# Performance work log

Hardware: AMD Instinct MI355X
Metric: run time of the kernel (lower is better)

Reference implementation:

```python
import jax, jax.numpy as jnp
import numpy as np

N = 50000      # nodes
E = 400000     # edges
G = 128        # graphs in batch
D_NODE = 64
EDGE_DIM = 72
HEADS = 4
H0, H1, H2 = 128, 128, 64
NC = 2
NEG = 0.2      # GATConv leaky_relu negative_slope default
D1 = H2 + EDGE_DIM - 1  # ffn input dim = 135


def _p(k, shape, s=0.1):
    return jax.random.normal(k, shape, dtype=jnp.float32) * s


def setup_inputs() -> dict:
    key = jax.random.key(0)
    ks = jax.random.split(key, 24)
    x = jax.random.normal(ks[0], (N, D_NODE), dtype=jnp.float32)
    edge_index = jax.random.randint(ks[1], (2, E), 0, N)
    edge_attr = jax.random.uniform(ks[2], (E, EDGE_DIM), dtype=jnp.float32)
    batch = jnp.sort(jax.random.randint(ks[3], (N,), 0, G))
    return dict(
        x=x, edge_index=edge_index, edge_attr=edge_attr, batch=batch,
        # GATConv layer 1: in=D_NODE, out=H0, heads=HEADS, concat
        W1=_p(ks[4], (D_NODE, HEADS * H0)), We1=_p(ks[5], (EDGE_DIM, HEADS * H0)),
        as1=_p(ks[6], (HEADS, H0)), ad1=_p(ks[7], (HEADS, H0)), ae1=_p(ks[8], (HEADS, H0)),
        b1=jnp.zeros((HEADS * H0,), jnp.float32),
        # GATConv layer 2: in=HEADS*H0, out=H1, heads=HEADS, concat
        W2=_p(ks[9], (HEADS * H0, HEADS * H1)), We2=_p(ks[10], (EDGE_DIM, HEADS * H1)),
        as2=_p(ks[11], (HEADS, H1)), ad2=_p(ks[12], (HEADS, H1)), ae2=_p(ks[13], (HEADS, H1)),
        b2=jnp.zeros((HEADS * H1,), jnp.float32),
        # GATConv layer 3: in=HEADS*H1, out=H2, heads=1, concat=False
        W3=_p(ks[14], (HEADS * H1, H2)), We3=_p(ks[15], (EDGE_DIM, H2)),
        as3=_p(ks[16], (1, H2)), ad3=_p(ks[17], (1, H2)), ae3=_p(ks[18], (1, H2)),
        b3=jnp.zeros((H2,), jnp.float32),
        # ffn: Linear(135 -> 67), ReLU, Linear(67 -> 2), Softmax
        Wf1=_p(ks[19], (D1, D1 // 2)), bf1=jnp.zeros((D1 // 2,), jnp.float32),
        Wf2=_p(ks[20], (D1 // 2, NC)), bf2=jnp.zeros((NC,), jnp.float32),
    )


def _seg_softmax(s, seg, n):
    # numerically-stable softmax over segments (per-destination neighborhoods)
    m = jax.ops.segment_max(s, seg, num_segments=n)
    m = jnp.where(jnp.isfinite(m), m, 0.0)
    e = jnp.exp(s - m[seg])
    z = jax.ops.segment_sum(e, seg, num_segments=n)
    return e / (z[seg] + 1e-16)


def _gat(x, src, dst, eattr, W, We, a_s, a_d, a_e, b, heads, oc, concat):
    # PyG GATConv with edge_dim: shared src/dst projection, edge feats only in attention
    n = x.shape[0]
    xs = (x @ W).reshape(n, heads, oc)            # [N,H,C]
    ee = (eattr @ We).reshape(-1, heads, oc)      # [Ea,H,C]
    alpha = (xs * a_s).sum(-1)[src] + (xs * a_d).sum(-1)[dst] + (ee * a_e).sum(-1)
    alpha = jax.nn.leaky_relu(alpha, NEG)         # [Ea,H]
    alpha = _seg_softmax(alpha, dst, n)
    out = jax.ops.segment_sum(xs[src] * alpha[:, :, None], dst, num_segments=n)
    out = out.reshape(n, heads * oc) if concat else out.mean(axis=1)
    return out + b


def reference(x, edge_index, edge_attr, batch,
              W1, We1, as1, ad1, ae1, b1,
              W2, We2, as2, ad2, ae2, b2,
              W3, We3, as3, ad3, ae3, b3,
              Wf1, bf1, Wf2, bf2):
    src, dst = edge_index[0], edge_index[1]
    n = x.shape[0]
    # --- 1-gram feature vector: scatter-add edge_attr[:, :-1] by graph of src ---
    eb = batch[src]
    og = jax.ops.segment_sum(edge_attr[:, :-1], eb, num_segments=G)   # [G, EDGE_DIM-1]
    og = og / jnp.maximum(jnp.linalg.norm(og, axis=1, keepdims=True), 1e-12)
    # --- add self loops, edge_attr fill_value='mean' (mean over incoming edges) ---
    ones_e = jnp.ones((src.shape[0],), x.dtype)
    deg = jax.ops.segment_sum(ones_e, dst, num_segments=n)
    loop_attr = jax.ops.segment_sum(edge_attr, dst, num_segments=n) / jnp.maximum(deg, 1.0)[:, None]
    nodes = jnp.arange(n)
    src_a = jnp.concatenate([src, nodes])
    dst_a = jnp.concatenate([dst, nodes])
    ea = jnp.concatenate([edge_attr, loop_attr], axis=0)
    # --- GAT stack with ReLU activations ---
    h = jax.nn.relu(_gat(x, src_a, dst_a, ea, W1, We1, as1, ad1, ae1, b1, HEADS, H0, True))
    h = jax.nn.relu(_gat(h, src_a, dst_a, ea, W2, We2, as2, ad2, ae2, b2, HEADS, H1, True))
    h = jax.nn.relu(_gat(h, src_a, dst_a, ea, W3, We3, as3, ad3, ae3, b3, 1, H2, False))
    # --- global mean pool over graphs ---
    cnt = jax.ops.segment_sum(jnp.ones((n,), x.dtype), batch, num_segments=G)
    pooled = jax.ops.segment_sum(h, batch, num_segments=G) / jnp.maximum(cnt, 1.0)[:, None]
    # --- concat + ffn (dropout p=0 in eval) + softmax ---
    z = jnp.concatenate([pooled, og], axis=1)                         # [G, 135]
    z = jax.nn.relu(z @ Wf1 + bf1)
    return jax.nn.softmax(z @ Wf2 + bf2, axis=1)
```

## Files before the change

kernel.cpp:

```cpp
#include <hip/hip_runtime.h>

#define NNODES 50000
#define NEDGES 400000
#define NEA    450000
#define NG     128
#define DEGCAP 96
#define OGW    72

typedef unsigned short u16;
typedef unsigned int   u32;
typedef __attribute__((ext_vector_type(8))) short short8v;
typedef __attribute__((ext_vector_type(4))) float f32x4;

static inline int ceil_div(int a, int b){ return (a + b - 1)/b; }

__device__ __forceinline__ u16 f2bf(float f){
  u32 u = __builtin_bit_cast(u32, f);
  u = (u + 0x7fffu + ((u >> 16) & 1u)) >> 16;
  return (u16)u;
}
__device__ __forceinline__ float bf2f(u16 b){
  return __builtin_bit_cast(float, (u32)b << 16);
}
__device__ __forceinline__ void gload_lds16(const u16* g, u16* l){
  __builtin_amdgcn_global_load_lds((const __attribute__((address_space(1))) void*)g,
                                   (__attribute__((address_space(3))) void*)l, 16, 0, 0);
}

__global__ void k_prep(const float* __restrict__ x, u16* __restrict__ xb,
                       const float* __restrict__ W1, u16* __restrict__ Wt1,
                       const float* __restrict__ W2, u16* __restrict__ Wt2,
                       const float* __restrict__ W3, u16* __restrict__ Wt3,
                       const float* __restrict__ We1, const float* __restrict__ ae1,
                       const float* __restrict__ We2, const float* __restrict__ ae2,
                       const float* __restrict__ We3, const float* __restrict__ ae3,
                       float* __restrict__ veall){
  int i = blockIdx.x*blockDim.x + threadIdx.x;
  if (i < 800000){
    float4 v = ((const float4*)x)[i];
    ((ushort4*)xb)[i] = make_ushort4(f2bf(v.x), f2bf(v.y), f2bf(v.z), f2bf(v.w));
    return;
  }
  i -= 800000;
  if (i < 32768){
    int n = i >> 6, k = i & 63;
    Wt1[i] = f2bf(W1[(size_t)k*512 + n]);
    return;
  }
  i -= 32768;
  if (i < 262144){
    int n = i >> 9, k = i & 511;
    Wt2[i] = f2bf(W2[(size_t)k*512 + n]);
    return;
  }
  i -= 262144;
  if (i < 32768){
    int n = i >> 9, k = i & 511;
    Wt3[i] = f2bf(W3[(size_t)k*64 + n]);
    return;
  }
  i -= 32768;
  if (i < 648){
    const float* We; const float* ae; int H, C, basej, li;
    if (i < 288){ We = We1; ae = ae1; H = 4; C = 128; basej = 0; li = i; }
    else if (i < 576){ We = We2; ae = ae2; H = 4; C = 128; basej = 4; li = i - 288; }
    else { We = We3; ae = ae3; H = 1; C = 64; basej = 8; li = i - 576; }
    int k = li / H, h = li - k*H;
    const float* wrow = We + (size_t)k*H*C + (size_t)h*C;
    const float* arow = ae + (size_t)h*C;
    float s = 0.f;
    for (int c = 0; c < C; ++c) s += wrow[c]*arow[c];
    veall[k*9 + basej + h] = s;
  }
}

__global__ void k_deg_gb(const int* __restrict__ src, const int* __restrict__ dst,
                         const int* __restrict__ batch,
                         int* __restrict__ deg, int* __restrict__ gb, int* __restrict__ gcnt){
  __shared__ int h[NG];
  int t = threadIdx.x;
  if (t < NG) h[t] = 0;
  __syncthreads();
  int e = blockIdx.x*blockDim.x + t;
  if (e < NEDGES){
    atomicAdd(&deg[dst[e]], 1);
    int g = batch[src[e]];
    gb[e] = g;
    atomicAdd(&h[g], 1);
  }
  __syncthreads();
  if (t < NG && h[t]) atomicAdd(&gcnt[t], h[t]);
}

__global__ __launch_bounds__(1024) void k_scans(const int* __restrict__ deg, int* __restrict__ off,
                                                const int* __restrict__ gcnt, int* __restrict__ goff,
                                                int* __restrict__ gcur){
  __shared__ int s[1024];
  int t = threadIdx.x;
  if (blockIdx.x == 0){
    const int CH = (NNODES + 1023)/1024;
    int i0 = t*CH, i1 = min(i0 + CH, NNODES);
    int loc = 0;
    for (int i = i0; i < i1; ++i) loc += deg[i] + 1;
    s[t] = loc; __syncthreads();
    for (int o = 1; o < 1024; o <<= 1){
      int v = (t >= o) ? s[t-o] : 0;
      __syncthreads();
      s[t] += v;
      __syncthreads();
    }
    int excl = s[t] - loc;
    for (int i = i0; i < i1; ++i){ off[i] = excl; excl += deg[i] + 1; }
    if (t == 1023) off[NNODES] = s[1023];
  } else {
    int v = 0;
    if (t < NG){ v = gcnt[t]; s[t] = v; }
    __syncthreads();
    for (int o = 1; o < NG; o <<= 1){
      int x = 0;
      if (t < NG && t >= o) x = s[t-o];
      __syncthreads();
      if (t < NG) s[t] += x;
      __syncthreads();
    }
    if (t < NG){ goff[t] = s[t] - v; gcur[t] = s[t] - v; }
  }
}

__global__ void k_scatter(const int* __restrict__ src, const int* __restrict__ dst,
                          const int* __restrict__ gb, const int* __restrict__ off,
                          int* __restrict__ cnt, int* __restrict__ gcur,
                          int* __restrict__ csr_src, int* __restrict__ csr_eid,
                          int* __restrict__ sortedeid){
  __shared__ int lcnt[NG];
  __shared__ int lbase[NG];
  int t = threadIdx.x;
  int e = blockIdx.x*256 + t;
  if (t < NG) lcnt[t] = 0;
  __syncthreads();
  int g = -1, lr = 0;
  if (e < NEDGES){
    int d = dst[e];
    int p = off[d] + atomicAdd(&cnt[d], 1);
    csr_src[p] = src[e];
    csr_eid[p] = e;
    g = gb[e];
    lr = atomicAdd(&lcnt[g], 1);
  } else {
    int n2 = e - NEDGES;
    if (n2 < NNODES){
      int p = off[n2+1] - 1;
      csr_src[p] = n2;
      csr_eid[p] = -1;
    }
  }
  __syncthreads();
  if (t < NG && lcnt[t]) lbase[t] = atomicAdd(&gcur[t], lcnt[t]);
  __syncthreads();
  if (g >= 0) sortedeid[lbase[g] + lr] = e;
}

__global__ __launch_bounds__(256) void k_og2(const float* __restrict__ attr,
    const int* __restrict__ goff, const int* __restrict__ gcnt,
    const int* __restrict__ sortedeid, float* __restrict__ og){
  __shared__ float red[16][OGW];
  int g = blockIdx.x >> 4, chunk = blockIdx.x & 15;
  int lane = threadIdx.x & 63, w = threadIdx.x >> 6;
  int esub = lane >> 4, l16 = lane & 15;
  int slot = w*4 + esub;
  int beg = goff[g], cnt = gcnt[g];
  int cbeg = beg + ((cnt*chunk) >> 4);
  int cend = beg + ((cnt*(chunk+1)) >> 4);
  f32x4 acc  = {0.f,0.f,0.f,0.f};
  f32x4 acch = {0.f,0.f,0.f,0.f};
  for (int i0 = cbeg; i0 < cend; i0 += 32){
    int e1 = i0 + slot, e2 = i0 + 16 + slot;
    int id1 = (e1 < cend) ? sortedeid[e1] : -1;
    int id2 = (e2 < cend) ? sortedeid[e2] : -1;
    f32x4 v1 = {0.f,0.f,0.f,0.f}, v2 = {0.f,0.f,0.f,0.f};
    f32x4 h1 = {0.f,0.f,0.f,0.f}, h2 = {0.f,0.f,0.f,0.f};
    if (id1 >= 0){
      v1 = *(const f32x4*)(attr + (size_t)id1*72 + l16*4);
      if (l16 < 2) h1 = *(const f32x4*)(attr + (size_t)id1*72 + 64 + l16*4);
    }
    if (id2 >= 0){
      v2 = *(const f32x4*)(attr + (size_t)id2*72 + l16*4);
      if (l16 < 2) h2 = *(const f32x4*)(attr + (size_t)id2*72 + 64 + l16*4);
    }
    acc += v1; acc += v2;
    if (l16 < 2){ acch += h1; acch += h2; }
  }
  #pragma unroll
  for (int j = 0; j < 4; ++j) red[slot][l16*4 + j] = acc[j];
  if (l16 < 2){
    #pragma unroll
    for (int j = 0; j < 4; ++j) red[slot][64 + l16*4 + j] = acch[j];
  }
  __syncthreads();
  int t = threadIdx.x;
  if (t < 71){
    float s = 0.f;
    #pragma unroll
    for (int q = 0; q < 16; ++q) s += red[q][t];
    atomicAdd(&og[g*OGW + t], s);
  }
}

__global__ __launch_bounds__(256) void k_se_all(const float* __restrict__ attr,
    const float* __restrict__ veall, float* __restrict__ se){
  __shared__ float vel[72*9];
  for (int i = threadIdx.x; i < 72*9; i += blockDim.x) vel[i] = veall[i];
  __syncthreads();
  int e = blockIdx.x*blockDim.x + threadIdx.x;
  if (e >= NEDGES) return;
  const float4* row = (const float4*)(attr + (size_t)e*72);
  float s[9];
  #pragma unroll
  for (int j = 0; j < 9; ++j) s[j] = 0.f;
  #pragma unroll
  for (int kk = 0; kk < 18; ++kk){
    float4 a = row[kk];
    #pragma unroll
    for (int j = 0; j < 9; ++j)
      s[j] += a.x*vel[(kk*4+0)*9+j] + a.y*vel[(kk*4+1)*9+j]
            + a.z*vel[(kk*4+2)*9+j] + a.w*vel[(kk*4+3)*9+j];
  }
  #pragma unroll
  for (int j = 0; j < 9; ++j) se[(size_t)e*9+j] = s[j];
}

__global__ __launch_bounds__(256) void k_gemm128(const u16* __restrict__ A,
    const u16* __restrict__ Bt, u16* __restrict__ C, int M, int K,
    const float* __restrict__ a_s, const float* __restrict__ a_d,
    float* __restrict__ ssrc, float* __restrict__ sdst){
  __shared__ __align__(16) u16 smem[128*128];
  u16* As = smem;
  u16* Bs = smem + 128*64;
  __shared__ float s_ps[128][2];
  __shared__ float s_pd[128][2];
  const int tid = threadIdx.x;
  const int wid = tid >> 6, lane = tid & 63;
  const int l15 = lane & 15, kslot = lane >> 4;
  const int wr = wid >> 1, wc = wid & 1;
  const int h = blockIdx.x;
  const int m0 = blockIdx.y * 128, n0 = h * 128;
  const int Nn = 512;
  f32x4 acc[4][4];
  #pragma unroll
  for (int mi = 0; mi < 4; ++mi)
    #pragma unroll
    for (int ni = 0; ni < 4; ++ni)
      acc[mi][ni] = (f32x4){0.f,0.f,0.f,0.f};

  for (int kt = 0; kt < K; kt += 64){
    #pragma unroll
    for (int r = 0; r < 4; ++r){
      int chunk = (r*4 + wid)*64 + lane;
      int row = chunk >> 3, c8 = chunk & 7;
      int srcc = c8 ^ (row & 7);
      int grow = m0 + row; if (grow > M-1) grow = M-1;
      gload_lds16(A + (size_t)grow*K + kt + srcc*8, &As[chunk*8]);
    }
    #pragma unroll
    for (int r = 0; r < 4; ++r){
      int chunk = (r*4 + wid)*64 + lane;
      int row = chunk >> 3, c8 = chunk & 7;
      int srcc = c8 ^ (row & 7);
      gload_lds16(Bt + (size_t)(n0+row)*K + kt + srcc*8, &Bs[chunk*8]);
    }
    __syncthreads();
    #pragma unroll
    for (int s = 0; s < 2; ++s){
      short8v a[4], b[4];
      #pragma unroll
      for (int mi = 0; mi < 4; ++mi){
        int row = wr*64 + mi*16 + l15;
        a[mi] = *(const short8v*)(&As[row*64 + (((s*4 + kslot) ^ (row&7))*8)]);
      }
      #pragma unroll
      for (int ni = 0; ni < 4; ++ni){
        int col = wc*64 + ni*16 + l15;
        b[ni] = *(const short8v*)(&Bs[col*64 + (((s*4 + kslot) ^ (col&7))*8)]);
      }
      #pragma unroll
      for (int mi = 0; mi < 4; ++mi)
        #pragma unroll
        for (int ni = 0; ni < 4; ++ni)
          acc[mi][ni] = __builtin_amdgcn_mfma_f32_16x16x32_bf16(a[mi], b[ni], acc[mi][ni], 0, 0, 0);
    }
    __syncthreads();
  }
  float asv[4], adv[4];
  #pragma unroll
  for (int ni = 0; ni < 4; ++ni){
    int c = wc*64 + ni*16 + l15;
    asv[ni] = a_s[h*128 + c];
    adv[ni] = a_d[h*128 + c];
  }
  #pragma unroll
  for (int mi = 0; mi < 4; ++mi){
    #pragma unroll
    for (int r = 0; r < 4; ++r){
      int row_l = wr*64 + mi*16 + kslot*4 + r;
      float ps = 0.f, pd = 0.f;
      #pragma unroll
      for (int ni = 0; ni < 4; ++ni){
        float v = acc[mi][ni][r];
        smem[row_l*128 + wc*64 + ni*16 + l15] = f2bf(v);
        ps += v*asv[ni];
        pd += v*adv[ni];
      }
      #pragma unroll
      for (int m = 8; m >= 1; m >>= 1){ ps += __shfl_xor(ps,m); pd += __shfl_xor(pd,m); }
      if (l15 == 0){ s_ps[row_l][wc] = ps; s_pd[row_l][wc] = pd; }
    }
  }
  __syncthreads();
  #pragma unroll
  for (int i = 0; i < 8; ++i){
    int c = i*256 + tid;
    int row = c >> 4, c16 = c & 15;
    int grow = m0 + row;
    if (grow < M)
      *(uint4*)(C + (size_t)grow*Nn + n0 + c16*8) = *(const uint4*)(&smem[row*128 + c16*8]);
  }
  if (tid < 128){
    int grow = m0 + tid;
    if (grow < M){
      ssrc[grow*4 + h] = s_ps[tid][0] + s_ps[tid][1];
      sdst[grow*4 + h] = s_pd[tid][0] + s_pd[tid][1];
    }
  }
}

__global__ __launch_bounds__(256) void k_gemm64(const u16* __restrict__ A,
    const u16* __restrict__ Bt, float* __restrict__ C, int M,
    const float* __restrict__ a_s, const float* __restrict__ a_d,
    float* __restrict__ ssrc, float* __restrict__ sdst){
  __shared__ __align__(16) u16 As[64*64];
  __shared__ __align__(16) u16 Bs[64*64];
  const int tid = threadIdx.x;
  const int wid = tid >> 6, lane = tid & 63;
  const int l15 = lane & 15, kslot = lane >> 4;
  const int m0 = blockIdx.x * 64;
  f32x4 acc[4];
  #pragma unroll
  for (int ni = 0; ni < 4; ++ni) acc[ni] = (f32x4){0.f,0.f,0.f,0.f};
  for (int kt = 0; kt < 512; kt += 64){
    #pragma unroll
    for (int r = 0; r < 2; ++r){
      int chunk = r*256 + tid;
      int row = chunk >> 3, c8 = chunk & 7;
      int srcc = c8 ^ (row & 7);
      int grow = m0 + row; if (grow > M-1) grow = M-1;
      gload_lds16(A + (size_t)grow*512 + kt + srcc*8, &As[chunk*8]);
    }
    #pragma unroll
    for (int r = 0; r < 2; ++r){
      int chunk = r*256 + tid;
      int row = chunk >> 3, c8 = chunk & 7;
      int srcc = c8 ^ (row & 7);
      gload_lds16(Bt + (size_t)row*512 + kt + srcc*8, &Bs[chunk*8]);
    }
    __syncthreads();
    #pragma unroll
    for (int s = 0; s < 2; ++s){
      int row = wid*16 + l15;
      short8v a = *(const short8v*)(&As[row*64 + (((s*4 + kslot) ^ (row&7))*8)]);
      #pragma unroll
      for (int ni = 0; ni < 4; ++ni){
        int col = ni*16 + l15;
        short8v b = *(const short8v*)(&Bs[col*64 + (((s*4 + kslot) ^ (col&7))*8)]);
        acc[ni] = __builtin_amdgcn_mfma_f32_16x16x32_bf16(a, b, acc[ni], 0, 0, 0);
      }
    }
    __syncthreads();
  }
  #pragma unroll
  for (int r = 0; r < 4; ++r){
    int grow = m0 + wid*16 + kslot*4 + r;
    float ps = 0.f, pd = 0.f;
    #pragma unroll
    for (int ni = 0; ni < 4; ++ni){
      float v = acc[ni][r];
      if (grow < M) C[(size_t)grow*64 + ni*16 + l15] = v;
      int c = ni*16 + l15;
      ps += v*a_s[c];
      pd += v*a_d[c];
    }
    #pragma unroll
    for (int m = 8; m >= 1; m >>= 1){ ps += __shfl_xor(ps,m); pd += __shfl_xor(pd,m); }
    if (l15 == 0 && grow < M){ ssrc[grow] = ps; sdst[grow] = pd; }
  }
}

__global__ __launch_bounds__(256) void k_agg12(const u16* __restrict__ xs,
    const int* __restrict__ off, const int* __restrict__ csr_src, const int* __restrict__ csr_eid,
    const float* __restrict__ ssrc, const float* __restrict__ sdst,
    const float* __restrict__ se, int soff,
    const float* __restrict__ bias, u16* __restrict__ out){
  __shared__ float s_al[4][DEGCAP][4];
  __shared__ int   s_col[4][DEGCAP];
  int w = threadIdx.x >> 6, lane = threadIdx.x & 63;
  int n = blockIdx.x*4 + w;
  int beg = off[n];
  int deg = off[n+1] - beg;
  if (deg > DEGCAP) deg = DEGCAP;
  int es = lane >> 2, h = lane & 3;
  float sd = sdst[n*4+h];
  float sesum = 0.f;
  for (int e0 = 0; e0 < deg-1; e0 += 16){
    int e = e0 + es;
    if (e < deg-1){
      int col = csr_src[beg+e];
      int eid = csr_eid[beg+e];
      float sr = se[(size_t)eid*9+soff+h];
      sesum += sr;
      float s = ssrc[col*4+h] + sd + sr;
      s = (s > 0.f) ? s : 0.2f*s;
      s_al[w][e][h] = s;
      if (h == 0) s_col[w][e] = col;
    }
  }
  #pragma unroll
  for (int msk = 4; msk < 64; msk <<= 1) sesum += __shfl_xor(sesum, msk);
  if (es == 0){
    float slp = sesum / fmaxf((float)(deg-1), 1.0f);
    float s = ssrc[n*4+h] + sd + slp;
    s = (s > 0.f) ? s : 0.2f*s;
    s_al[w][deg-1][h] = s;
    if (h == 0) s_col[w][deg-1] = n;
  }
  float m = -1e30f;
  for (int e = es; e < deg; e += 16) m = fmaxf(m, s_al[w][e][h]);
  #pragma unroll
  for (int msk = 4; msk < 64; msk <<= 1) m = fmaxf(m, __shfl_xor(m, msk));
  float z = 0.f;
  for (int e = es; e < deg; e += 16){ float ex = expf(s_al[w][e][h]-m); s_al[w][e][h] = ex; z += ex; }
  #pragma unroll
  for (int msk = 4; msk < 64; msk <<= 1) z += __shfl_xor(z, msk);
  float inv = 1.0f/(z + 1e-16f);
  for (int e = es; e < deg; e += 16) s_al[w][e][h] *= inv;
  __syncthreads();
  int hh = lane >> 4;
  f32x4 accA = {0.f,0.f,0.f,0.f}, accB = {0.f,0.f,0.f,0.f};
  short8v v = *(const short8v*)(xs + (size_t)s_col[w][0]*512 + lane*8);
  for (int e = 0; e < deg; ++e){
    short8v vn = (short8v){0,0,0,0,0,0,0,0};
    if (e+1 < deg) vn = *(const short8v*)(xs + (size_t)s_col[w][e+1]*512 + lane*8);
    float a = s_al[w][e][hh];
    accA[0] += a*bf2f((u16)v[0]); accA[1] += a*bf2f((u16)v[1]);
    accA[2] += a*bf2f((u16)v[2]); accA[3] += a*bf2f((u16)v[3]);
    accB[0] += a*bf2f((u16)v[4]); accB[1] += a*bf2f((u16)v[5]);
    accB[2] += a*bf2f((u16)v[6]); accB[3] += a*bf2f((u16)v[7]);
    v = vn;
  }
  f32x4 b0 = *(const f32x4*)(bias + lane*8);
  f32x4 b1 = *(const f32x4*)(bias + lane*8 + 4);
  short8v res;
  res[0] = (short)f2bf(fmaxf(accA[0]+b0[0], 0.f));
  res[1] = (short)f2bf(fmaxf(accA[1]+b0[1], 0.f));
  res[2] = (short)f2bf(fmaxf(accA[2]+b0[2], 0.f));
  res[3] = (short)f2bf(fmaxf(accA[3]+b0[3], 0.f));
  res[4] = (short)f2bf(fmaxf(accB[0]+b1[0], 0.f));
  res[5] = (short)f2bf(fmaxf(accB[1]+b1[1], 0.f));
  res[6] = (short)f2bf(fmaxf(accB[2]+b1[2], 0.f));
  res[7] = (short)f2bf(fmaxf(accB[3]+b1[3], 0.f));
  *(short8v*)(out + (size_t)n*512 + lane*8) = res;
}

__global__ __launch_bounds__(256) void k_agg3(const float* __restrict__ xs,
    const int* __restrict__ off, const int* __restrict__ csr_src, const int* __restrict__ csr_eid,
    const float* __restrict__ ssrc, const float* __restrict__ sdst,
    const float* __restrict__ se,
    const float* __restrict__ bias, float* __restrict__ out){
  __shared__ float s_al[4][DEGCAP];
  __shared__ int   s_col[4][DEGCAP];
  int w = threadIdx.x >> 6, lane = threadIdx.x & 63;
  int n = blockIdx.x*4 + w;
  int beg = off[n];
  int deg = off[n+1] - beg;
  if (deg > DEGCAP) deg = DEGCAP;
  float sd = sdst[n];
  float sesum = 0.f;
  for (int e0 = 0; e0 < deg-1; e0 += 64){
    int e = e0 + lane;
    if (e < deg-1){
      int col = csr_src[beg+e];
      int eid = csr_eid[beg+e];
      float sr = se[(size_t)eid*9+8];
      sesum += sr;
      float s = ssrc[col] + sd + sr;
      s = (s > 0.f) ? s : 0.2f*s;
      s_al[w][e] = s;
      s_col[w][e] = col;
    }
  }
  #pragma unroll
  for (int msk = 1; msk < 64; msk <<= 1) sesum += __shfl_xor(sesum, msk);
  if (lane == 0){
    float slp = sesum / fmaxf((float)(deg-1), 1.0f);
    float s = ssrc[n] + sd + slp;
    s = (s > 0.f) ? s : 0.2f*s;
    s_al[w][deg-1] = s;
    s_col[w][deg-1] = n;
  }
  float m = -1e30f;
  for (int e = lane; e < deg; e += 64) m = fmaxf(m, s_al[w][e]);
  #pragma unroll
  for (int msk = 1; msk < 64; msk <<= 1) m = fmaxf(m, __shfl_xor(m, msk));
  float z = 0.f;
  for (int e = lane; e < deg; e += 64){ float ex = expf(s_al[w][e]-m); s_al[w][e] = ex; z += ex; }
  #pragma unroll
  for (int msk = 1; msk < 64; msk <<= 1) z += __shfl_xor(z, msk);
  float inv = 1.0f/(z + 1e-16f);
  for (int e = lane; e < deg; e += 64) s_al[w][e] *= inv;
  __syncthreads();
  float acc = 0.f;
  float v = xs[(size_t)s_col[w][0]*64 + lane];
  for (int e = 0; e < deg; ++e){
    float vn = 0.f;
    if (e+1 < deg) vn = xs[(size_t)s_col[w][e+1]*64 + lane];
    acc += s_al[w][e] * v;
    v = vn;
  }
  out[(size_t)n*64 + lane] = fmaxf(acc + bias[lane], 0.f);
}

__global__ __launch_bounds__(64) void k_pool(const float* __restrict__ h, const int* __restrict__ batch,
                                             float* __restrict__ pooled, int* __restrict__ cntg){
  int l = threadIdx.x;
  int start = blockIdx.x * 128;
  if (start >= NNODES) return;
  int endn = min(start + 128, NNODES);
  float acc = 0.f;
  int curg = batch[start];
  int run = 0;
  for (int n = start; n < endn; ++n){
    int g = batch[n];
    if (g != curg){
      atomicAdd(&pooled[curg*64+l], acc);
      if (l == 0) atomicAdd(&cntg[curg], run);
      acc = 0.f; run = 0; curg = g;
    }
    acc += h[(size_t)n*64 + l];
    ++run;
  }
  atomicAdd(&pooled[curg*64+l], acc);
  if (l == 0) atomicAdd(&cntg[curg], run);
}

__global__ void k_ffn(const float* __restrict__ pooled, const int* __restrict__ cntg,
                      const float* __restrict__ og,
                      const float* __restrict__ Wf1, const float* __restrict__ bf1,
                      const float* __restrict__ Wf2, const float* __restrict__ bf2,
                      float* __restrict__ out){
  __shared__ float z[135];
  __shared__ float z1[67];
  __shared__ float o2[2];
  int g = blockIdx.x, t = threadIdx.x;
  if (t < 64) z[t] = pooled[g*64+t] * (1.0f/fmaxf((float)cntg[g], 1.0f));
  else if (t < 135) z[t] = og[g*OGW + (t-64)];
  __syncthreads();
  if (t == 0){
    float s = 0.f;
    for (int k = 0; k < 71; ++k) s += z[64+k]*z[64+k];
    float scale = 1.0f / fmaxf(sqrtf(s), 1e-12f);
    for (int k = 0; k < 71; ++k) z[64+k] *= scale;
  }
  __syncthreads();
  if (t < 67){
    float s = bf1[t];
    for (int d = 0; d < 135; ++d) s += z[d]*Wf1[d*67+t];
    z1[t] = fmaxf(s, 0.f);
  }
  __syncthreads();
  if (t < 2){
    float s = bf2[t];
    for (int j = 0; j < 67; ++j) s += z1[j]*Wf2[j*2+t];
    o2[t] = s;
  }
  __syncthreads();
  if (t == 0){
    float m = fmaxf(o2[0], o2[1]);
    float e0 = expf(o2[0]-m), e1 = expf(o2[1]-m);
    float inv = 1.0f/(e0+e1);
    out[g*2+0] = e0*inv;
    out[g*2+1] = e1*inv;
  }
}

extern "C" void kernel_launch(void* const* d_in, const int* in_sizes, int n_in,
                              void* d_out, int out_size, void* d_ws, size_t ws_size,
                              hipStream_t stream){
  const float* x     = (const float*)d_in[0];
  const int*   ei    = (const int*)d_in[1];
  const float* eattr = (const float*)d_in[2];
  const int*   batch = (const int*)d_in[3];
  const float* W1  = (const float*)d_in[4];
  const float* We1 = (const float*)d_in[5];
  const float* as1 = (const float*)d_in[6];
  const float* ad1 = (const float*)d_in[7];
  const float* ae1 = (const float*)d_in[8];
  const float* b1  = (const float*)d_in[9];
  const float* W2  = (const float*)d_in[10];
  const float* We2 = (const float*)d_in[11];
  const float* as2 = (const float*)d_in[12];
  const float* ad2 = (const float*)d_in[13];
  const float* ae2 = (const float*)d_in[14];
  const float* b2  = (const float*)d_in[15];
  const float* W3  = (const float*)d_in[16];
  const float* We3 = (const float*)d_in[17];
  const float* as3 = (const float*)d_in[18];
  const float* ad3 = (const float*)d_in[19];
  const float* ae3 = (const float*)d_in[20];
  const float* b3  = (const float*)d_in[21];
  const float* Wf1 = (const float*)d_in[22];
  const float* bf1 = (const float*)d_in[23];
  const float* Wf2 = (const float*)d_in[24];
  const float* bf2 = (const float*)d_in[25];
  (void)in_sizes; (void)n_in; (void)out_size; (void)ws_size;
  const int* src = ei;
  const int* dst = ei + NEDGES;
  float* out = (float*)d_out;

  char* base = (char*)d_ws;
  size_t woff = 0;
  auto alloc = [&](size_t bytes)->char*{
    char* p = base + woff;
    woff += (bytes + 255) & ~(size_t)255;
    return p;
  };
  u16*   xsb    = (u16*)  alloc((size_t)NNODES*512*2);
  u16*   hb     = (u16*)  alloc((size_t)NNODES*512*2);
  float* xs3    = (float*)alloc((size_t)NNODES*64*4);
  float* h3     = (float*)alloc((size_t)NNODES*64*4);
  u16*   xb     = (u16*)  alloc((size_t)NNODES*64*2);
  u16*   Wt1    = (u16*)  alloc((size_t)512*64*2);
  u16*   Wt2    = (u16*)  alloc((size_t)512*512*2);
  u16*   Wt3    = (u16*)  alloc((size_t)64*512*2);
  float* se     = (float*)alloc((size_t)NEDGES*9*4);
  float* ssrc   = (float*)alloc((size_t)NNODES*4*4);
  float* sdst   = (float*)alloc((size_t)NNODES*4*4);
  float* veall  = (float*)alloc(72*9*4);
  int*   gb     = (int*)alloc((size_t)NEDGES*4);
  int*   csroff = (int*)alloc((size_t)(NNODES+1)*4);
  int*   csrsrc = (int*)alloc((size_t)NEA*4);
  int*   csreid = (int*)alloc((size_t)NEA*4);
  int*   goff   = (int*)alloc(NG*4);
  int*   gcur   = (int*)alloc(NG*4);
  int*   sortedeid = (int*)alloc((size_t)NEDGES*4);
  size_t z0 = woff;
  int*   deg    = (int*)alloc((size_t)NNODES*4);
  int*   cnt    = (int*)alloc((size_t)NNODES*4);
  int*   gcnt   = (int*)alloc(NG*4);
  float* og     = (float*)alloc((size_t)NG*OGW*4);
  float* pooled = (float*)alloc((size_t)NG*64*4);
  int*   cntg   = (int*)alloc((size_t)NG*4);
  size_t zlen = woff - z0;

  hipMemsetAsync(base + z0, 0, zlen, stream);

  k_prep<<<ceil_div(800000+32768+262144+32768+648,256),256,0,stream>>>(
      x, xb, W1, Wt1, W2, Wt2, W3, Wt3, We1, ae1, We2, ae2, We3, ae3, veall);

  k_deg_gb <<<ceil_div(NEDGES,256),256,0,stream>>>(src, dst, batch, deg, gb, gcnt);
  k_scans  <<<2,1024,0,stream>>>(deg, csroff, gcnt, goff, gcur);
  k_scatter<<<ceil_div(NEDGES+NNODES,256),256,0,stream>>>(src, dst, gb, csroff, cnt, gcur,
                                                          csrsrc, csreid, sortedeid);

  k_og2   <<<NG*16,256,0,stream>>>(eattr, goff, gcnt, sortedeid, og);
  k_se_all<<<ceil_div(NEDGES,256),256,0,stream>>>(eattr, veall, se);

  dim3 g128(4, ceil_div(NNODES,128));

  k_gemm128<<<g128,256,0,stream>>>(xb, Wt1, xsb, NNODES, 64, as1, ad1, ssrc, sdst);
  k_agg12<<<NNODES/4,256,0,stream>>>(xsb, csroff, csrsrc, csreid, ssrc, sdst, se, 0, b1, hb);

  k_gemm128<<<g128,256,0,stream>>>(hb, Wt2, xsb, NNODES, 512, as2, ad2, ssrc, sdst);
  k_agg12<<<NNODES/4,256,0,stream>>>(xsb, csroff, csrsrc, csreid, ssrc, sdst, se, 4, b2, hb);

  k_gemm64<<<ceil_div(NNODES,64),256,0,stream>>>(hb, Wt3, xs3, NNODES, as3, ad3, ssrc, sdst);
  k_agg3<<<NNODES/4,256,0,stream>>>(xs3, csroff, csrsrc, csreid, ssrc, sdst, se, b3, h3);

  k_pool<<<ceil_div(NNODES,128),64,0,stream>>>(h3, batch, pooled, cntg);
  k_ffn <<<NG,192,0,stream>>>(pooled, cntg, og, Wf1, bf1, Wf2, bf2, out);
}
```

Measured before the change: 609.1 us.

## Store edge scores in CSR order, bf16 layer-3 features, batched gathers in aggregation

The per-edge attention score projections are now written directly in CSR order, split into per-layer arrays. This removes the csr_eid indirection and the scattered 9-wide reads in each aggregation kernel. The layer-3 GEMM now emits bf16 features via an LDS staging pass, halving the bytes gathered in k_agg3. The aggregation loops are unrolled by 4 edges with padded neighbour lists and use __expf, exposing more independent gathers in flight. In exchange, the padding costs extra loads of the node's own row, and layer 3 loses some precision.

```diff
diff --git a/kernel.cpp b/kernel.cpp
--- a/kernel.cpp
+++ b/kernel.cpp
@@ -19,9 +19,8 @@
   u = (u + 0x7fffu + ((u >> 16) & 1u)) >> 16;
   return (u16)u;
 }
-__device__ __forceinline__ float bf2f(u16 b){
-  return __builtin_bit_cast(float, (u32)b << 16);
-}
+__device__ __forceinline__ float bfLO(u32 q){ return __builtin_bit_cast(float, q << 16); }
+__device__ __forceinline__ float bfHI(u32 q){ return __builtin_bit_cast(float, q & 0xffff0000u); }
 __device__ __forceinline__ void gload_lds16(const u16* g, u16* l){
   __builtin_amdgcn_global_load_lds((const __attribute__((address_space(1))) void*)g,
                                    (__attribute__((address_space(3))) void*)l, 16, 0, 0);
@@ -130,7 +129,7 @@
 __global__ void k_scatter(const int* __restrict__ src, const int* __restrict__ dst,
                           const int* __restrict__ gb, const int* __restrict__ off,
                           int* __restrict__ cnt, int* __restrict__ gcur,
-                          int* __restrict__ csr_src, int* __restrict__ csr_eid,
+                          int* __restrict__ csr_src, int* __restrict__ edgepos,
                           int* __restrict__ sortedeid){
   __shared__ int lcnt[NG];
   __shared__ int lbase[NG];
@@ -143,7 +142,7 @@
     int d = dst[e];
     int p = off[d] + atomicAdd(&cnt[d], 1);
     csr_src[p] = src[e];
-    csr_eid[p] = e;
+    edgepos[e] = p;
     g = gb[e];
     lr = atomicAdd(&lcnt[g], 1);
   } else {
@@ -151,7 +150,6 @@
     if (n2 < NNODES){
       int p = off[n2+1] - 1;
       csr_src[p] = n2;
-      csr_eid[p] = -1;
     }
   }
   __syncthreads();
@@ -207,7 +205,8 @@
 }
 
 __global__ __launch_bounds__(256) void k_se_all(const float* __restrict__ attr,
-    const float* __restrict__ veall, float* __restrict__ se){
+    const int* __restrict__ edgepos, const float* __restrict__ veall,
+    float* __restrict__ se1, float* __restrict__ se2, float* __restrict__ se3){
   __shared__ float vel[72*9];
   for (int i = threadIdx.x; i < 72*9; i += blockDim.x) vel[i] = veall[i];
   __syncthreads();
@@ -225,8 +224,10 @@
       s[j] += a.x*vel[(kk*4+0)*9+j] + a.y*vel[(kk*4+1)*9+j]
             + a.z*vel[(kk*4+2)*9+j] + a.w*vel[(kk*4+3)*9+j];
   }
-  #pragma unroll
-  for (int j = 0; j < 9; ++j) se[(size_t)e*9+j] = s[j];
+  int p = edgepos[e];
+  *(float4*)(se1 + (size_t)p*4) = make_float4(s[0], s[1], s[2], s[3]);
+  *(float4*)(se2 + (size_t)p*4) = make_float4(s[4], s[5], s[6], s[7]);
+  se3[p] = s[8];
 }
 
 __global__ __launch_bounds__(256) void k_gemm128(const u16* __restrict__ A,
@@ -334,7 +335,7 @@
 }
 
 __global__ __launch_bounds__(256) void k_gemm64(const u16* __restrict__ A,
-    const u16* __restrict__ Bt, float* __restrict__ C, int M,
+    const u16* __restrict__ Bt, u16* __restrict__ C, int M,
     const float* __restrict__ a_s, const float* __restrict__ a_d,
     float* __restrict__ ssrc, float* __restrict__ sdst){
   __shared__ __align__(16) u16 As[64*64];
@@ -378,13 +379,14 @@
   }
   #pragma unroll
   for (int r = 0; r < 4; ++r){
-    int grow = m0 + wid*16 + kslot*4 + r;
+    int row_l = wid*16 + kslot*4 + r;
+    int grow = m0 + row_l;
     float ps = 0.f, pd = 0.f;
     #pragma unroll
     for (int ni = 0; ni < 4; ++ni){
       float v = acc[ni][r];
-      if (grow < M) C[(size_t)grow*64 + ni*16 + l15] = v;
       int c = ni*16 + l15;
+      As[row_l*64 + c] = f2bf(v);
       ps += v*a_s[c];
       pd += v*a_d[c];
     }
@@ -392,12 +394,21 @@
     for (int m = 8; m >= 1; m >>= 1){ ps += __shfl_xor(ps,m); pd += __shfl_xor(pd,m); }
     if (l15 == 0 && grow < M){ ssrc[grow] = ps; sdst[grow] = pd; }
   }
+  __syncthreads();
+  #pragma unroll
+  for (int i = 0; i < 2; ++i){
+    int c = i*256 + tid;
+    int row = c >> 3, c8 = c & 7;
+    int grow = m0 + row;
+    if (grow < M)
+      *(uint4*)(C + (size_t)grow*64 + c8*8) = *(const uint4*)(&As[row*64 + c8*8]);
+  }
 }
 
 __global__ __launch_bounds__(256) void k_agg12(const u16* __restrict__ xs,
-    const int* __restrict__ off, const int* __restrict__ csr_src, const int* __restrict__ csr_eid,
+    const int* __restrict__ off, const int* __restrict__ csr_src,
     const float* __restrict__ ssrc, const float* __restrict__ sdst,
-    const float* __restrict__ se, int soff,
+    const float* __restrict__ sep,
     const float* __restrict__ bias, u16* __restrict__ out){
   __shared__ float s_al[4][DEGCAP][4];
   __shared__ int   s_col[4][DEGCAP];
@@ -413,8 +424,7 @@
     int e = e0 + es;
     if (e < deg-1){
       int col = csr_src[beg+e];
-      int eid = csr_eid[beg+e];
-      float sr = se[(size_t)eid*9+soff+h];
+      float sr = sep[(size_t)(beg+e)*4 + h];
       sesum += sr;
       float s = ssrc[col*4+h] + sd + sr;
       s = (s > 0.f) ? s : 0.2f*s;
@@ -436,24 +446,32 @@
   #pragma unroll
   for (int msk = 4; msk < 64; msk <<= 1) m = fmaxf(m, __shfl_xor(m, msk));
   float z = 0.f;
-  for (int e = es; e < deg; e += 16){ float ex = expf(s_al[w][e][h]-m); s_al[w][e][h] = ex; z += ex; }
+  for (int e = es; e < deg; e += 16){ float ex = __expf(s_al[w][e][h]-m); s_al[w][e][h] = ex; z += ex; }
   #pragma unroll
   for (int msk = 4; msk < 64; msk <<= 1) z += __shfl_xor(z, msk);
   float inv = 1.0f/(z + 1e-16f);
   for (int e = es; e < deg; e += 16) s_al[w][e][h] *= inv;
+  int degR = (deg + 3) & ~3;
+  for (int e = deg + es; e < degR; e += 16){ s_al[w][e][h] = 0.f; if (h == 0) s_col[w][e] = n; }
   __syncthreads();
   int hh = lane >> 4;
   f32x4 accA = {0.f,0.f,0.f,0.f}, accB = {0.f,0.f,0.f,0.f};
-  short8v v = *(const short8v*)(xs + (size_t)s_col[w][0]*512 + lane*8);
-  for (int e = 0; e < deg; ++e){
-    short8v vn = (short8v){0,0,0,0,0,0,0,0};
-    if (e+1 < deg) vn = *(const short8v*)(xs + (size_t)s_col[w][e+1]*512 + lane*8);
-    float a = s_al[w][e][hh];
-    accA[0] += a*bf2f((u16)v[0]); accA[1] += a*bf2f((u16)v[1]);
-    accA[2] += a*bf2f((u16)v[2]); accA[3] += a*bf2f((u16)v[3]);
-    accB[0] += a*bf2f((u16)v[4]); accB[1] += a*bf2f((u16)v[5]);
-    accB[2] += a*bf2f((u16)v[6]); accB[3] += a*bf2f((u16)v[7]);
-    v = vn;
+  for (int e = 0; e < degR; e += 4){
+    int c0 = s_col[w][e+0], c1 = s_col[w][e+1], c2 = s_col[w][e+2], c3 = s_col[w][e+3];
+    uint4 q0 = *(const uint4*)(xs + (size_t)c0*512 + lane*8);
+    uint4 q1 = *(const uint4*)(xs + (size_t)c1*512 + lane*8);
+    uint4 q2 = *(const uint4*)(xs + (size_t)c2*512 + lane*8);
+    uint4 q3 = *(const uint4*)(xs + (size_t)c3*512 + lane*8);
+    float a0 = s_al[w][e+0][hh], a1 = s_al[w][e+1][hh];
+    float a2 = s_al[w][e+2][hh], a3 = s_al[w][e+3][hh];
+    accA[0] += a0*bfLO(q0.x) + a1*bfLO(q1.x) + a2*bfLO(q2.x) + a3*bfLO(q3.x);
+    accA[1] += a0*bfHI(q0.x) + a1*bfHI(q1.x) + a2*bfHI(q2.x) + a3*bfHI(q3.x);
+    accA[2] += a0*bfLO(q0.y) + a1*bfLO(q1.y) + a2*bfLO(q2.y) + a3*bfLO(q3.y);
+    accA[3] += a0*bfHI(q0.y) + a1*bfHI(q1.y) + a2*bfHI(q2.y) + a3*bfHI(q3.y);
+    accB[0] += a0*bfLO(q0.z) + a1*bfLO(q1.z) + a2*bfLO(q2.z) + a3*bfLO(q3.z);
+    accB[1] += a0*bfHI(q0.z) + a1*bfHI(q1.z) + a2*bfHI(q2.z) + a3*bfHI(q3.z);
+    accB[2] += a0*bfLO(q0.w) + a1*bfLO(q1.w) + a2*bfLO(q2.w) + a3*bfLO(q3.w);
+    accB[3] += a0*bfHI(q0.w) + a1*bfHI(q1.w) + a2*bfHI(q2.w) + a3*bfHI(q3.w);
   }
   f32x4 b0 = *(const f32x4*)(bias + lane*8);
   f32x4 b1 = *(const f32x4*)(bias + lane*8 + 4);
@@ -469,10 +487,10 @@
   *(short8v*)(out + (size_t)n*512 + lane*8) = res;
 }
 
-__global__ __launch_bounds__(256) void k_agg3(const float* __restrict__ xs,
-    const int* __restrict__ off, const int* __restrict__ csr_src, const int* __restrict__ csr_eid,
+__global__ __launch_bounds__(256) void k_agg3(const u16* __restrict__ xs,
+    const int* __restrict__ off, const int* __restrict__ csr_src,
     const float* __restrict__ ssrc, const float* __restrict__ sdst,
-    const float* __restrict__ se,
+    const float* __restrict__ se3,
     const float* __restrict__ bias, float* __restrict__ out){
   __shared__ float s_al[4][DEGCAP];
   __shared__ int   s_col[4][DEGCAP];
@@ -487,8 +505,7 @@
     int e = e0 + lane;
     if (e < deg-1){
       int col = csr_src[beg+e];
-      int eid = csr_eid[beg+e];
-      float sr = se[(size_t)eid*9+8];
+      float sr = se3[beg+e];
       sesum += sr;
       float s = ssrc[col] + sd + sr;
       s = (s > 0.f) ? s : 0.2f*s;
@@ -510,21 +527,32 @@
   #pragma unroll
   for (int msk = 1; msk < 64; msk <<= 1) m = fmaxf(m, __shfl_xor(m, msk));
   float z = 0.f;
-  for (int e = lane; e < deg; e += 64){ float ex = expf(s_al[w][e]-m); s_al[w][e] = ex; z += ex; }
+  for (int e = lane; e < deg; e += 64){ float ex = __expf(s_al[w][e]-m); s_al[w][e] = ex; z += ex; }
   #pragma unroll
   for (int msk = 1; msk < 64; msk <<= 1) z += __shfl_xor(z, msk);
   float inv = 1.0f/(z + 1e-16f);
   for (int e = lane; e < deg; e += 64) s_al[w][e] *= inv;
-  __syncthreads();
-  float acc = 0.f;
-  float v = xs[(size_t)s_col[w][0]*64 + lane];
-  for (int e = 0; e < deg; ++e){
-    float vn = 0.f;
-    if (e+1 < deg) vn = xs[(size_t)s_col[w][e+1]*64 + lane];
-    acc += s_al[w][e] * v;
-    v = vn;
-  }
-  out[(size_t)n*64 + lane] = fmaxf(acc + bias[lane], 0.f);
+  int degR = (deg + 3) & ~3;
+  for (int e = deg + lane; e < degR; e += 64){ s_al[w][e] = 0.f; s_col[w][e] = n; }
+  __syncthreads();
+  int half = lane >> 5, cp = lane & 31;
+  float a0 = 0.f, a1 = 0.f;
+  for (int e = 0; e < degR; e += 4){
+    int c0 = s_col[w][e + half], c1 = s_col[w][e + 2 + half];
+    u32 q0 = *(const u32*)(xs + (size_t)c0*64 + cp*2);
+    u32 q1 = *(const u32*)(xs + (size_t)c1*64 + cp*2);
+    float al0 = s_al[w][e + half], al1 = s_al[w][e + 2 + half];
+    a0 += al0*bfLO(q0) + al1*bfLO(q1);
+    a1 += al0*bfHI(q0) + al1*bfHI(q1);
+  }
+  a0 += __shfl_xor(a0, 32);
+  a1 += __shfl_xor(a1, 32);
+  if (half == 0){
+    float2 o;
+    o.x = fmaxf(a0 + bias[cp*2+0], 0.f);
+    o.y = fmaxf(a1 + bias[cp*2+1], 0.f);
+    *(float2*)(out + (size_t)n*64 + cp*2) = o;
+  }
 }
 
 __global__ __launch_bounds__(64) void k_pool(const float* __restrict__ h, const int* __restrict__ batch,
@@ -633,20 +661,22 @@
   };
   u16*   xsb    = (u16*)  alloc((size_t)NNODES*512*2);
   u16*   hb     = (u16*)  alloc((size_t)NNODES*512*2);
-  float* xs3    = (float*)alloc((size_t)NNODES*64*4);
+  u16*   xs3b   = (u16*)  alloc((size_t)NNODES*64*2);
   float* h3     = (float*)alloc((size_t)NNODES*64*4);
   u16*   xb     = (u16*)  alloc((size_t)NNODES*64*2);
   u16*   Wt1    = (u16*)  alloc((size_t)512*64*2);
   u16*   Wt2    = (u16*)  alloc((size_t)512*512*2);
   u16*   Wt3    = (u16*)  alloc((size_t)64*512*2);
-  float* se     = (float*)alloc((size_t)NEDGES*9*4);
+  float* se1    = (float*)alloc((size_t)NEA*4*4);
+  float* se2    = (float*)alloc((size_t)NEA*4*4);
+  float* se3    = (float*)alloc((size_t)NEA*4);
   float* ssrc   = (float*)alloc((size_t)NNODES*4*4);
   float* sdst   = (float*)alloc((size_t)NNODES*4*4);
   float* veall  = (float*)alloc(72*9*4);
   int*   gb     = (int*)alloc((size_t)NEDGES*4);
   int*   csroff = (int*)alloc((size_t)(NNODES+1)*4);
   int*   csrsrc = (int*)alloc((size_t)NEA*4);
-  int*   csreid = (int*)alloc((size_t)NEA*4);
+  int*   edgepos= (int*)alloc((size_t)NEDGES*4);
   int*   goff   = (int*)alloc(NG*4);
   int*   gcur   = (int*)alloc(NG*4);
   int*   sortedeid = (int*)alloc((size_t)NEDGES*4);
@@ -667,21 +697,21 @@
   k_deg_gb <<<ceil_div(NEDGES,256),256,0,stream>>>(src, dst, batch, deg, gb, gcnt);
   k_scans  <<<2,1024,0,stream>>>(deg, csroff, gcnt, goff, gcur);
   k_scatter<<<ceil_div(NEDGES+NNODES,256),256,0,stream>>>(src, dst, gb, csroff, cnt, gcur,
-                                                          csrsrc, csreid, sortedeid);
+                                                          csrsrc, edgepos, sortedeid);
 
   k_og2   <<<NG*16,256,0,stream>>>(eattr, goff, gcnt, sortedeid, og);
-  k_se_all<<<ceil_div(NEDGES,256),256,0,stream>>>(eattr, veall, se);
+  k_se_all<<<ceil_div(NEDGES,256),256,0,stream>>>(eattr, edgepos, veall, se1, se2, se3);
 
   dim3 g128(4, ceil_div(NNODES,128));
 
   k_gemm128<<<g128,256,0,stream>>>(xb, Wt1, xsb, NNODES, 64, as1, ad1, ssrc, sdst);
-  k_agg12<<<NNODES/4,256,0,stream>>>(xsb, csroff, csrsrc, csreid, ssrc, sdst, se, 0, b1, hb);
+  k_agg12<<<NNODES/4,256,0,stream>>>(xsb, csroff, csrsrc, ssrc, sdst, se1, b1, hb);
 
   k_gemm128<<<g128,256,0,stream>>>(hb, Wt2, xsb, NNODES, 512, as2, ad2, ssrc, sdst);
-  k_agg12<<<NNODES/4,256,0,stream>>>(xsb, csroff, csrsrc, csreid, ssrc, sdst, se, 4, b2, hb);
-
-  k_gemm64<<<ceil_div(NNODES,64),256,0,stream>>>(hb, Wt3, xs3, NNODES, as3, ad3, ssrc, sdst);
-  k_agg3<<<NNODES/4,256,0,stream>>>(xs3, csroff, csrsrc, csreid, ssrc, sdst, se, b3, h3);
+  k_agg12<<<NNODES/4,256,0,stream>>>(xsb, csroff, csrsrc, ssrc, sdst, se2, b2, hb);
+
+  k_gemm64<<<ceil_div(NNODES,64),256,0,stream>>>(hb, Wt3, xs3b, NNODES, as3, ad3, ssrc, sdst);
+  k_agg3<<<NNODES/4,256,0,stream>>>(xs3b, csroff, csrsrc, ssrc, sdst, se3, b3, h3);
 
   k_pool<<<ceil_div(NNODES,128),64,0,stream>>>(h3, batch, pooled, cntg);
   k_ffn <<<NG,192,0,stream>>>(pooled, cntg, og, Wf1, bf1, Wf2, bf2, out);
```

After: 600.8 us. Within noise of the previous version (-1.4%).
